# Kernel tuning notes

Hardware: AMD Instinct MI355X
Metric: run time of the kernel (lower is better)

Reference implementation:

```python
import jax, jax.numpy as jnp
import numpy as np

F = 256          # in_features
T = 8            # num_fragment_ion_types = 4 types * 2 charges
N_MONO, N_CLEAV, N_FRAG, N_OUT = 150000, 100000, 80000, 40000
D_CLEAV, D_JOIN, D_COMB = 4, 2, 4


def setup_inputs() -> dict:
    key = jax.random.key(0)
    ks = jax.random.split(key, 14)
    s = 0.05
    return {
        "feature": jax.random.normal(ks[0], (N_MONO, F), jnp.float32),
        "Wg_lost": jax.random.normal(ks[1], (F, 1), jnp.float32) * s,
        "Wg_ret": jax.random.normal(ks[2], (F, 1), jnp.float32) * s,
        "W_ih": jax.random.normal(ks[3], (4 * F, 2 * F), jnp.float32) * s,
        "W_hh": jax.random.normal(ks[4], (4 * F, F), jnp.float32) * s,
        "b_ih": jax.random.normal(ks[5], (4 * F,), jnp.float32) * s,
        "b_hh": jax.random.normal(ks[6], (4 * F,), jnp.float32) * s,
        "Wg_frag": jax.random.normal(ks[7], (F, 1), jnp.float32) * s,
        "W_out": jax.random.normal(ks[8], (F, T), jnp.float32) * s,
        "b_out": jnp.zeros((T,), jnp.float32),
        "lost_src": jax.random.randint(ks[9], (N_CLEAV, D_CLEAV), 0, N_MONO),
        "retained_src": jax.random.randint(ks[10], (N_CLEAV, D_CLEAV), 0, N_MONO),
        "join_src": jax.random.randint(ks[11], (N_FRAG, D_JOIN), 0, N_CLEAV),
        "combine_src": jax.random.randint(ks[12], (N_OUT, D_COMB), 0, N_FRAG),
    }


def _attention_sum(h, Wg):
    # h: [N, D, F] mailbox; gate = Linear(F,1,no bias); softmax over neighbor axis
    logits = jnp.einsum('ndf,fo->ndo', h, Wg)          # [N, D, 1]
    a = jax.nn.softmax(logits, axis=1)
    return jnp.sum(a * h, axis=1)                       # [N, F]


def _lstm(x, W_ih, W_hh, b_ih, b_hh):
    # x: [N, L, I]; torch nn.LSTM gate order i,f,g,o; zero initial state
    N = x.shape[0]
    H = W_hh.shape[1]
    def step(carry, xt):
        h, c = carry
        gates = xt @ W_ih.T + h @ W_hh.T + b_ih + b_hh  # [N, 4H]
        i, f, g, o = jnp.split(gates, 4, axis=-1)
        c = jax.nn.sigmoid(f) * c + jax.nn.sigmoid(i) * jnp.tanh(g)
        h = jax.nn.sigmoid(o) * jnp.tanh(c)
        return (h, c), h
    init = (jnp.zeros((N, H), x.dtype), jnp.zeros((N, H), x.dtype))
    _, hs = jax.lax.scan(step, init, jnp.swapaxes(x, 0, 1))
    return jnp.swapaxes(hs, 0, 1)                       # [N, L, H]


def reference(feature, Wg_lost, Wg_ret, W_ih, W_hh, b_ih, b_hh,
              Wg_frag, W_out, b_out,
              lost_src, retained_src, join_src, combine_src):
    h_lost = _attention_sum(feature[lost_src], Wg_lost)        # [N_cleav, F]
    h_ret = _attention_sum(feature[retained_src], Wg_ret)      # [N_cleav, F]
    cleav = jnp.concatenate([h_lost, h_ret], axis=-1)          # [N_cleav, 2F]
    # Fragment pull over 'join' edges: LSTM over neighbor set, then attention sum
    hs = _lstm(cleav[join_src], W_ih, W_hh, b_ih, b_hh)        # [N_frag, D_join, F]
    frag = _attention_sum(hs, Wg_frag)                         # [N_frag, F]
    # Output head: Linear + ReLU
    frag_out = jax.nn.relu(frag @ W_out + b_out)               # [N_frag, T]
    # copy_u_sum over 'combine' edges: scatter-sum of src outputs to dst
    return frag_out[combine_src].sum(axis=1)                   # [N_out, T]
```

## Files before the change

### kernel.cpp

```cpp
#include <hip/hip_runtime.h>

typedef unsigned short u16;
typedef unsigned int u32;
typedef float f32x4 __attribute__((ext_vector_type(4)));
typedef __bf16 bf16x8 __attribute__((ext_vector_type(8)));

#define F 256
#define T_OUT 8
#define N_MONO 150000
#define N_CLEAV 100000
#define N_FRAG 80000
#define N_OUT 40000
#define M_CLEAV_PAD 100352

static __device__ __forceinline__ u16 f2bf(float f) {
  u32 u = __float_as_uint(f);
  u32 r = (u + 0x7FFFu + ((u >> 16) & 1u)) >> 16;
  return (u16)r;
}
static __device__ __forceinline__ float bf2f(u16 b) {
  return __uint_as_float(((u32)b) << 16);
}
static __device__ __forceinline__ float sigmoidf(float x) {
  return __frcp_rn(1.0f + __expf(-x));
}
static __device__ __forceinline__ float fast_tanh(float x) {
  return 1.0f - 2.0f * __frcp_rn(__expf(2.0f * x) + 1.0f);
}
static __device__ __forceinline__ void async_copy16(const u16* g, const u16* l) {
  __builtin_amdgcn_global_load_lds(
      (const __attribute__((address_space(1))) u32*)g,
      (__attribute__((address_space(3))) u32*)l,
      16, 0, 0);
}

__global__ __launch_bounds__(256) void prep_kernel(
    const float* __restrict__ Wih, const float* __restrict__ Whh,
    const float* __restrict__ bih, const float* __restrict__ bhh,
    u16* __restrict__ Wihb, u16* __restrict__ Whhb, float* __restrict__ bias) {
  int i = blockIdx.x * 256 + threadIdx.x;
  if (i < 1024 * 512) Wihb[i] = f2bf(Wih[i]);
  if (i < 1024 * 256) Whhb[i] = f2bf(Whh[i]);
  if (i < 1024) bias[i] = bih[i] + bhh[i];
}

__global__ __launch_bounds__(256) void attn_pull(
    const float* __restrict__ feat, const float* __restrict__ WgL,
    const float* __restrict__ WgR, const int* __restrict__ lostS,
    const int* __restrict__ retS, u16* __restrict__ cleav) {
  int wave = threadIdx.x >> 6, lane = threadIdx.x & 63;
  int n = blockIdx.x * 4 + wave;
  if (n >= N_CLEAV) return;
  const float4 wgl = *(const float4*)(WgL + lane * 4);
  const float4 wgr = *(const float4*)(WgR + lane * 4);
  for (int sg = 0; sg < 2; ++sg) {
    const int* src = sg ? retS : lostS;
    float4 wg = sg ? wgr : wgl;
    int4 ridx = *(const int4*)(src + n * 4);
    int r[4] = {ridx.x, ridx.y, ridx.z, ridx.w};
    float4 x[4];
#pragma unroll
    for (int d = 0; d < 4; ++d)
      x[d] = *(const float4*)(feat + (size_t)r[d] * F + lane * 4);
    float logit[4];
#pragma unroll
    for (int d = 0; d < 4; ++d) {
      float p = x[d].x * wg.x + x[d].y * wg.y + x[d].z * wg.z + x[d].w * wg.w;
#pragma unroll
      for (int off = 32; off; off >>= 1) p += __shfl_xor(p, off);
      logit[d] = p;
    }
    float mx = fmaxf(fmaxf(logit[0], logit[1]), fmaxf(logit[2], logit[3]));
    float e0 = __expf(logit[0] - mx), e1 = __expf(logit[1] - mx);
    float e2 = __expf(logit[2] - mx), e3 = __expf(logit[3] - mx);
    float inv = 1.f / (e0 + e1 + e2 + e3);
    float a0 = e0 * inv, a1 = e1 * inv, a2 = e2 * inv, a3 = e3 * inv;
    float4 acc;
    acc.x = a0 * x[0].x + a1 * x[1].x + a2 * x[2].x + a3 * x[3].x;
    acc.y = a0 * x[0].y + a1 * x[1].y + a2 * x[2].y + a3 * x[3].y;
    acc.z = a0 * x[0].z + a1 * x[1].z + a2 * x[2].z + a3 * x[3].z;
    acc.w = a0 * x[0].w + a1 * x[1].w + a2 * x[2].w + a3 * x[3].w;
    u32 lo = (u32)f2bf(acc.x) | ((u32)f2bf(acc.y) << 16);
    u32 hi = (u32)f2bf(acc.z) | ((u32)f2bf(acc.w) << 16);
    *(uint2*)(cleav + (size_t)n * 512 + sg * 256 + lane * 4) = make_uint2(lo, hi);
  }
}

template <int EPI, int K>
__global__ __launch_bounds__(512, 2) void gemm256(
    const u16* __restrict__ A, const u16* __restrict__ Bw,
    u16* __restrict__ C, const float* __restrict__ bias,
    int nper, int mstrips_valid) {
  __shared__ u16 sh[2][32768];
  const int flat = blockIdx.x;
  const int xcd = flat & 7;
  const int w = flat >> 3;
  const int mstrip = xcd * nper + (w >> 2);
  const int nstrip = w & 3;
  if (mstrip >= mstrips_valid) return;
  const int m0 = mstrip * 256;
  const int n0 = nstrip * 256;

  const int tid = threadIdx.x;
  const int lane = tid & 63;
  const int wave = tid >> 6;
  const int quad = lane >> 4;
  const int l16 = lane & 15;
  const int s7 = l16 & 7;
  const int wm2 = wave >> 2;
  const int wn4 = wave & 3;

  const int arow = (wm2 * 128 + l16) * 64;
  const int brow = 16384 + (wn4 * 64 + l16) * 64;
  const int coff0 = ((0 + quad) ^ s7) * 8;
  const int coff1 = ((4 + quad) ^ s7) * 8;

  int srow[2], ssw[2], sdst[2];
#pragma unroll
  for (int j = 0; j < 2; j++) {
    int c = j * 512 + tid;
    int r = c >> 3, p = c & 7;
    srow[j] = r;
    ssw[j] = (p ^ (r & 7)) * 8;
    sdst[j] = (j * 512 + (tid & ~63)) * 8;
  }
  const u16* Abase = A + (size_t)m0 * K;
  const u16* Bbase = Bw + (size_t)n0 * K;

  auto stage = [&](int buf, int mat, int h, int kt) {
    const u16* gb = (mat ? Bbase : Abase) + (size_t)(h * 128) * K + kt * 64;
    const u16* lb = &sh[buf][mat * 16384 + h * 8192];
#pragma unroll
    for (int j = 0; j < 2; j++)
      async_copy16(gb + (size_t)srow[j] * K + ssw[j], lb + sdst[j]);
  };

  f32x4 acc[8][4];
#pragma unroll
  for (int i = 0; i < 8; i++)
#pragma unroll
    for (int j = 0; j < 4; j++) acc[i][j] = (f32x4){0.f, 0.f, 0.f, 0.f};

  constexpr int nK = K / 64;
  stage(0, 0, 0, 0); stage(0, 0, 1, 0); stage(0, 1, 0, 0); stage(0, 1, 1, 0);
  if (nK > 1) { stage(1, 1, 0, 1); stage(1, 1, 1, 1); }
  __builtin_amdgcn_s_waitcnt(0xF74);
  __builtin_amdgcn_s_barrier();

  bf16x8 a[4][2], b0[2][2], b1[2][2];
#pragma unroll
  for (int t = 0; t < nK; ++t) {
    const int bsel = t & 1;
    const u16* S = &sh[bsel][0];

#pragma unroll
    for (int i = 0; i < 4; i++) {
      a[i][0] = *(const bf16x8*)&S[arow + i * 1024 + coff0];
      a[i][1] = *(const bf16x8*)&S[arow + i * 1024 + coff1];
    }
#pragma unroll
    for (int j = 0; j < 2; j++) {
      b0[j][0] = *(const bf16x8*)&S[brow + j * 1024 + coff0];
      b0[j][1] = *(const bf16x8*)&S[brow + j * 1024 + coff1];
    }
    if (t + 1 < nK) stage(bsel ^ 1, 0, 0, t + 1);
    __builtin_amdgcn_s_waitcnt(0xC87F);
    __builtin_amdgcn_s_barrier();
    __builtin_amdgcn_s_waitcnt(0xC07F);
    __builtin_amdgcn_sched_barrier(0);
    __builtin_amdgcn_s_setprio(1);
#pragma unroll
    for (int i = 0; i < 4; i++)
#pragma unroll
      for (int j = 0; j < 2; j++) {
        acc[i][j] = __builtin_amdgcn_mfma_f32_16x16x32_bf16(a[i][0], b0[j][0], acc[i][j], 0, 0, 0);
        acc[i][j] = __builtin_amdgcn_mfma_f32_16x16x32_bf16(a[i][1], b0[j][1], acc[i][j], 0, 0, 0);
      }
    __builtin_amdgcn_s_setprio(0);
    __builtin_amdgcn_s_barrier();

#pragma unroll
    for (int j = 0; j < 2; j++) {
      b1[j][0] = *(const bf16x8*)&S[brow + (2 + j) * 1024 + coff0];
      b1[j][1] = *(const bf16x8*)&S[brow + (2 + j) * 1024 + coff1];
    }
    if (t + 1 < nK) stage(bsel ^ 1, 0, 1, t + 1);
    __builtin_amdgcn_s_barrier();
    __builtin_amdgcn_s_waitcnt(0xC07F);
    __builtin_amdgcn_sched_barrier(0);
    __builtin_amdgcn_s_setprio(1);
#pragma unroll
    for (int i = 0; i < 4; i++)
#pragma unroll
      for (int j = 0; j < 2; j++) {
        acc[i][2 + j] = __builtin_amdgcn_mfma_f32_16x16x32_bf16(a[i][0], b1[j][0], acc[i][2 + j], 0, 0, 0);
        acc[i][2 + j] = __builtin_amdgcn_mfma_f32_16x16x32_bf16(a[i][1], b1[j][1], acc[i][2 + j], 0, 0, 0);
      }
    __builtin_amdgcn_s_setprio(0);
    __builtin_amdgcn_s_barrier();

#pragma unroll
    for (int i = 0; i < 4; i++) {
      a[i][0] = *(const bf16x8*)&S[arow + (4 + i) * 1024 + coff0];
      a[i][1] = *(const bf16x8*)&S[arow + (4 + i) * 1024 + coff1];
    }
    if (t + 2 < nK) stage(bsel, 1, 0, t + 2);
    __builtin_amdgcn_s_barrier();
    __builtin_amdgcn_s_waitcnt(0xC07F);
    __builtin_amdgcn_sched_barrier(0);
    __builtin_amdgcn_s_setprio(1);
#pragma unroll
    for (int i = 0; i < 4; i++)
#pragma unroll
      for (int j = 0; j < 2; j++) {
        acc[4 + i][j] = __builtin_amdgcn_mfma_f32_16x16x32_bf16(a[i][0], b0[j][0], acc[4 + i][j], 0, 0, 0);
        acc[4 + i][j] = __builtin_amdgcn_mfma_f32_16x16x32_bf16(a[i][1], b0[j][1], acc[4 + i][j], 0, 0, 0);
      }
    __builtin_amdgcn_s_setprio(0);
    __builtin_amdgcn_s_barrier();

    if (t + 2 < nK) stage(bsel, 1, 1, t + 2);
    __builtin_amdgcn_s_barrier();
    __builtin_amdgcn_s_setprio(1);
#pragma unroll
    for (int i = 0; i < 4; i++)
#pragma unroll
      for (int j = 0; j < 2; j++) {
        acc[4 + i][2 + j] = __builtin_amdgcn_mfma_f32_16x16x32_bf16(a[i][0], b1[j][0], acc[4 + i][2 + j], 0, 0, 0);
        acc[4 + i][2 + j] = __builtin_amdgcn_mfma_f32_16x16x32_bf16(a[i][1], b1[j][1], acc[4 + i][2 + j], 0, 0, 0);
      }
    __builtin_amdgcn_s_setprio(0);
    if (t + 2 < nK) __builtin_amdgcn_s_waitcnt(0xF74);
    else            __builtin_amdgcn_s_waitcnt(0xF70);
    __builtin_amdgcn_s_barrier();
  }

  float badd[4];
#pragma unroll
  for (int j = 0; j < 4; j++)
    badd[j] = (EPI == 0) ? bias[n0 + wn4 * 64 + j * 16 + l16] : 0.f;
#pragma unroll
  for (int i = 0; i < 8; i++) {
    const int mrow = m0 + wm2 * 128 + i * 16 + quad * 4;
#pragma unroll
    for (int j = 0; j < 4; j++) {
      const int n = n0 + wn4 * 64 + j * 16 + l16;
#pragma unroll
      for (int r = 0; r < 4; r++)
        C[(size_t)(mrow + r) * 1024 + n] = f2bf(acc[i][j][r] + badd[j]);
    }
  }
}

__global__ __launch_bounds__(256) void lstm_step1(
    const u16* __restrict__ P, const int* __restrict__ join,
    u16* __restrict__ h1, u16* __restrict__ c1) {
  int wave = threadIdx.x >> 6, lane = threadIdx.x & 63;
  int m = blockIdx.x * 4 + wave;
  if (m >= N_FRAG) return;
  int j0 = join[2 * m];
  const u16* row = P + (size_t)j0 * 1024 + lane * 4;
  ushort4 iv = *(const ushort4*)(row);
  ushort4 gv = *(const ushort4*)(row + 512);
  ushort4 ov = *(const ushort4*)(row + 768);
  const u16* ivp = (const u16*)&iv;
  const u16* gvp = (const u16*)&gv;
  const u16* ovp = (const u16*)&ov;
  ushort4 h4, c4;
  u16* h4p = (u16*)&h4;
  u16* c4p = (u16*)&c4;
#pragma unroll
  for (int k = 0; k < 4; k++) {
    float c = sigmoidf(bf2f(ivp[k])) * fast_tanh(bf2f(gvp[k]));
    float hv = sigmoidf(bf2f(ovp[k])) * fast_tanh(c);
    h4p[k] = f2bf(hv);
    c4p[k] = f2bf(c);
  }
  *(ushort4*)(h1 + (size_t)m * 256 + lane * 4) = h4;
  *(ushort4*)(c1 + (size_t)m * 256 + lane * 4) = c4;
}

__global__ __launch_bounds__(256) void lstm_step2_attn_out(
    const u16* __restrict__ G2, const u16* __restrict__ P,
    const int* __restrict__ join, const u16* __restrict__ c1,
    const u16* __restrict__ h1b, const float* __restrict__ Wg,
    const float* __restrict__ Wout, const float* __restrict__ bout,
    float* __restrict__ frag_out) {
  int wave = threadIdx.x >> 6, lane = threadIdx.x & 63;
  int m = blockIdx.x * 4 + wave;
  if (m >= N_FRAG) return;
  int j1 = join[2 * m + 1];
  const u16* row = G2 + (size_t)m * 1024 + lane * 4;
  const u16* prow = P + (size_t)j1 * 1024 + lane * 4;
  ushort4 iv = *(const ushort4*)(row);
  ushort4 fv = *(const ushort4*)(row + 256);
  ushort4 gv = *(const ushort4*)(row + 512);
  ushort4 ov = *(const ushort4*)(row + 768);
  ushort4 pi = *(const ushort4*)(prow);
  ushort4 pf = *(const ushort4*)(prow + 256);
  ushort4 pg = *(const ushort4*)(prow + 512);
  ushort4 po = *(const ushort4*)(prow + 768);
  ushort4 c4 = *(const ushort4*)(c1 + (size_t)m * 256 + lane * 4);
  ushort4 h4 = *(const ushort4*)(h1b + (size_t)m * 256 + lane * 4);
  float4 wg = *(const float4*)(Wg + lane * 4);
  const u16* ivp = (const u16*)&iv; const u16* pip = (const u16*)&pi;
  const u16* fvp = (const u16*)&fv; const u16* pfp = (const u16*)&pf;
  const u16* gvp = (const u16*)&gv; const u16* pgp = (const u16*)&pg;
  const u16* ovp = (const u16*)&ov; const u16* pop = (const u16*)&po;
  const u16* c4p = (const u16*)&c4;
  const u16* h4p = (const u16*)&h4;
  const float* wgp = (const float*)&wg;

  float h1v[4], h2v[4];
  float p1 = 0.f, p2 = 0.f;
#pragma unroll
  for (int k = 0; k < 4; k++) {
    float gi = bf2f(ivp[k]) + bf2f(pip[k]);
    float gf = bf2f(fvp[k]) + bf2f(pfp[k]);
    float gg = bf2f(gvp[k]) + bf2f(pgp[k]);
    float go = bf2f(ovp[k]) + bf2f(pop[k]);
    float c2 = sigmoidf(gf) * bf2f(c4p[k]) + sigmoidf(gi) * fast_tanh(gg);
    float h2 = sigmoidf(go) * fast_tanh(c2);
    h2v[k] = h2;
    h1v[k] = bf2f(h4p[k]);
    p1 += h1v[k] * wgp[k];
    p2 += h2 * wgp[k];
  }
#pragma unroll
  for (int off = 32; off; off >>= 1) {
    p1 += __shfl_xor(p1, off);
    p2 += __shfl_xor(p2, off);
  }
  float mx = fmaxf(p1, p2);
  float e1 = __expf(p1 - mx), e2 = __expf(p2 - mx);
  float inv = __frcp_rn(e1 + e2);
  float a1 = e1 * inv, a2 = e2 * inv;

  float acc[8];
#pragma unroll
  for (int t = 0; t < 8; t++) acc[t] = 0.f;
#pragma unroll
  for (int k = 0; k < 4; k++) {
    float frag = a1 * h1v[k] + a2 * h2v[k];
    int h = lane * 4 + k;
    float4 w0 = *(const float4*)(Wout + h * 8);
    float4 w1 = *(const float4*)(Wout + h * 8 + 4);
    acc[0] += frag * w0.x; acc[1] += frag * w0.y;
    acc[2] += frag * w0.z; acc[3] += frag * w0.w;
    acc[4] += frag * w1.x; acc[5] += frag * w1.y;
    acc[6] += frag * w1.z; acc[7] += frag * w1.w;
  }
#pragma unroll
  for (int off = 32; off; off >>= 1)
#pragma unroll
    for (int t = 0; t < 8; t++) acc[t] += __shfl_xor(acc[t], off);
  if (lane == 0) {
    float4 o0, o1;
    o0.x = fmaxf(acc[0] + bout[0], 0.f);
    o0.y = fmaxf(acc[1] + bout[1], 0.f);
    o0.z = fmaxf(acc[2] + bout[2], 0.f);
    o0.w = fmaxf(acc[3] + bout[3], 0.f);
    o1.x = fmaxf(acc[4] + bout[4], 0.f);
    o1.y = fmaxf(acc[5] + bout[5], 0.f);
    o1.z = fmaxf(acc[6] + bout[6], 0.f);
    o1.w = fmaxf(acc[7] + bout[7], 0.f);
    *(float4*)(frag_out + (size_t)m * 8) = o0;
    *(float4*)(frag_out + (size_t)m * 8 + 4) = o1;
  }
}

__global__ __launch_bounds__(256) void scatter_sum(
    const float* __restrict__ frag_out, const int* __restrict__ comb,
    float* __restrict__ out) {
  int tid = blockIdx.x * 256 + threadIdx.x;
  if (tid >= N_OUT * 8) return;
  int n = tid >> 3, t = tid & 7;
  float s = 0.f;
#pragma unroll
  for (int d = 0; d < 4; d++) {
    int f = comb[n * 4 + d];
    s += frag_out[(size_t)f * 8 + t];
  }
  out[tid] = s;
}

extern "C" void kernel_launch(void* const* d_in, const int* in_sizes, int n_in,
                              void* d_out, int out_size, void* d_ws, size_t ws_size,
                              hipStream_t stream) {
  const float* feature = (const float*)d_in[0];
  const float* WgL = (const float*)d_in[1];
  const float* WgR = (const float*)d_in[2];
  const float* Wih = (const float*)d_in[3];
  const float* Whh = (const float*)d_in[4];
  const float* bih = (const float*)d_in[5];
  const float* bhh = (const float*)d_in[6];
  const float* Wgf = (const float*)d_in[7];
  const float* Wout = (const float*)d_in[8];
  const float* bout = (const float*)d_in[9];
  const int* lostS = (const int*)d_in[10];
  const int* retS = (const int*)d_in[11];
  const int* joinS = (const int*)d_in[12];
  const int* combS = (const int*)d_in[13];
  float* out = (float*)d_out;

  char* ws = (char*)d_ws;
  size_t off = 0;
  auto alloc = [&](size_t bytes) -> char* {
    char* p = ws + off;
    off = (off + bytes + 255) & ~(size_t)255;
    return p;
  };
  u16* Wihb = (u16*)alloc((size_t)1024 * 512 * 2);
  u16* Whhb = (u16*)alloc((size_t)1024 * 256 * 2);
  float* bias = (float*)alloc(1024 * 4);
  u16* P = (u16*)alloc((size_t)M_CLEAV_PAD * 1024 * 2);
  u16* h1 = (u16*)alloc((size_t)N_FRAG * 256 * 2);
  u16* c1 = (u16*)alloc((size_t)N_FRAG * 256 * 2);
  float* frag_out = (float*)alloc((size_t)N_FRAG * 8 * 4);
  char* uni = alloc((size_t)M_CLEAV_PAD * 1024 * 2);
  u16* cleav = (u16*)uni;
  u16* gates2 = (u16*)uni;

  prep_kernel<<<2048, 256, 0, stream>>>(Wih, Whh, bih, bhh, Wihb, Whhb, bias);
  attn_pull<<<N_CLEAV / 4, 256, 0, stream>>>(feature, WgL, WgR, lostS, retS, cleav);
  gemm256<0, 512><<<1568, 512, 0, stream>>>(cleav, Wihb, P, bias, 49, 392);
  lstm_step1<<<N_FRAG / 4, 256, 0, stream>>>(P, joinS, h1, c1);
  gemm256<1, 256><<<1280, 512, 0, stream>>>(h1, Whhb, gates2, nullptr, 40, 313);
  lstm_step2_attn_out<<<N_FRAG / 4, 256, 0, stream>>>(
      gates2, P, joinS, c1, h1, Wgf, Wout, bout, frag_out);
  scatter_sum<<<(N_OUT * 8 + 255) / 256, 256, 0, stream>>>(frag_out, combS, out);
}
```

Baseline: 683.5 us.

## Precompute per-node gate logits and bf16 feature copy before attention gather

```diff
diff --git a/kernel.cpp b/kernel.cpp
--- a/kernel.cpp
+++ b/kernel.cpp
@@ -44,44 +44,65 @@
   if (i < 1024) bias[i] = bih[i] + bhh[i];
 }
 
-__global__ __launch_bounds__(256) void attn_pull(
+__global__ __launch_bounds__(256) void feat_prep(
     const float* __restrict__ feat, const float* __restrict__ WgL,
-    const float* __restrict__ WgR, const int* __restrict__ lostS,
-    const int* __restrict__ retS, u16* __restrict__ cleav) {
+    const float* __restrict__ WgR, u16* __restrict__ featb,
+    float* __restrict__ glog) {
+  int wave = threadIdx.x >> 6, lane = threadIdx.x & 63;
+  int n = blockIdx.x * 4 + wave;
+  if (n >= N_MONO) return;
+  float4 x = *(const float4*)(feat + (size_t)n * F + lane * 4);
+  u32 lo = (u32)f2bf(x.x) | ((u32)f2bf(x.y) << 16);
+  u32 hi = (u32)f2bf(x.z) | ((u32)f2bf(x.w) << 16);
+  *(uint2*)(featb + (size_t)n * F + lane * 4) = make_uint2(lo, hi);
+  float4 wl = *(const float4*)(WgL + lane * 4);
+  float4 wr = *(const float4*)(WgR + lane * 4);
+  float pl = x.x * wl.x + x.y * wl.y + x.z * wl.z + x.w * wl.w;
+  float pr = x.x * wr.x + x.y * wr.y + x.z * wr.z + x.w * wr.w;
+#pragma unroll
+  for (int off = 32; off; off >>= 1) {
+    pl += __shfl_xor(pl, off);
+    pr += __shfl_xor(pr, off);
+  }
+  if (lane == 0) {
+    glog[n * 2] = pl;
+    glog[n * 2 + 1] = pr;
+  }
+}
+
+__global__ __launch_bounds__(256) void attn_pull2(
+    const u16* __restrict__ featb, const float* __restrict__ glog,
+    const int* __restrict__ lostS, const int* __restrict__ retS,
+    u16* __restrict__ cleav) {
   int wave = threadIdx.x >> 6, lane = threadIdx.x & 63;
   int n = blockIdx.x * 4 + wave;
   if (n >= N_CLEAV) return;
-  const float4 wgl = *(const float4*)(WgL + lane * 4);
-  const float4 wgr = *(const float4*)(WgR + lane * 4);
+#pragma unroll
   for (int sg = 0; sg < 2; ++sg) {
     const int* src = sg ? retS : lostS;
-    float4 wg = sg ? wgr : wgl;
     int4 ridx = *(const int4*)(src + n * 4);
     int r[4] = {ridx.x, ridx.y, ridx.z, ridx.w};
-    float4 x[4];
-#pragma unroll
-    for (int d = 0; d < 4; ++d)
-      x[d] = *(const float4*)(feat + (size_t)r[d] * F + lane * 4);
-    float logit[4];
+    ushort4 x4[4];
+    float lg[4];
 #pragma unroll
     for (int d = 0; d < 4; ++d) {
-      float p = x[d].x * wg.x + x[d].y * wg.y + x[d].z * wg.z + x[d].w * wg.w;
-#pragma unroll
-      for (int off = 32; off; off >>= 1) p += __shfl_xor(p, off);
-      logit[d] = p;
-    }
-    float mx = fmaxf(fmaxf(logit[0], logit[1]), fmaxf(logit[2], logit[3]));
-    float e0 = __expf(logit[0] - mx), e1 = __expf(logit[1] - mx);
-    float e2 = __expf(logit[2] - mx), e3 = __expf(logit[3] - mx);
-    float inv = 1.f / (e0 + e1 + e2 + e3);
-    float a0 = e0 * inv, a1 = e1 * inv, a2 = e2 * inv, a3 = e3 * inv;
-    float4 acc;
-    acc.x = a0 * x[0].x + a1 * x[1].x + a2 * x[2].x + a3 * x[3].x;
-    acc.y = a0 * x[0].y + a1 * x[1].y + a2 * x[2].y + a3 * x[3].y;
-    acc.z = a0 * x[0].z + a1 * x[1].z + a2 * x[2].z + a3 * x[3].z;
-    acc.w = a0 * x[0].w + a1 * x[1].w + a2 * x[2].w + a3 * x[3].w;
-    u32 lo = (u32)f2bf(acc.x) | ((u32)f2bf(acc.y) << 16);
-    u32 hi = (u32)f2bf(acc.z) | ((u32)f2bf(acc.w) << 16);
+      x4[d] = *(const ushort4*)(featb + (size_t)r[d] * F + lane * 4);
+      lg[d] = glog[r[d] * 2 + sg];
+    }
+    float mx = fmaxf(fmaxf(lg[0], lg[1]), fmaxf(lg[2], lg[3]));
+    float e0 = __expf(lg[0] - mx), e1 = __expf(lg[1] - mx);
+    float e2 = __expf(lg[2] - mx), e3 = __expf(lg[3] - mx);
+    float inv = __frcp_rn(e0 + e1 + e2 + e3);
+    float a[4] = {e0 * inv, e1 * inv, e2 * inv, e3 * inv};
+    float acc[4] = {0.f, 0.f, 0.f, 0.f};
+#pragma unroll
+    for (int d = 0; d < 4; ++d) {
+      const u16* xp = (const u16*)&x4[d];
+#pragma unroll
+      for (int k = 0; k < 4; k++) acc[k] += a[d] * bf2f(xp[k]);
+    }
+    u32 lo = (u32)f2bf(acc[0]) | ((u32)f2bf(acc[1]) << 16);
+    u32 hi = (u32)f2bf(acc[2]) | ((u32)f2bf(acc[3]) << 16);
     *(uint2*)(cleav + (size_t)n * 512 + sg * 256 + lane * 4) = make_uint2(lo, hi);
   }
 }
@@ -420,9 +441,12 @@
   char* uni = alloc((size_t)M_CLEAV_PAD * 1024 * 2);
   u16* cleav = (u16*)uni;
   u16* gates2 = (u16*)uni;
+  u16* featb = P;
+  float* glog = (float*)(P + (size_t)N_MONO * F);
 
   prep_kernel<<<2048, 256, 0, stream>>>(Wih, Whh, bih, bhh, Wihb, Whhb, bias);
-  attn_pull<<<N_CLEAV / 4, 256, 0, stream>>>(feature, WgL, WgR, lostS, retS, cleav);
+  feat_prep<<<(N_MONO + 3) / 4, 256, 0, stream>>>(feature, WgL, WgR, featb, glog);
+  attn_pull2<<<N_CLEAV / 4, 256, 0, stream>>>(featb, glog, lostS, retS, cleav);
   gemm256<0, 512><<<1568, 512, 0, stream>>>(cleav, Wihb, P, bias, 49, 392);
   lstm_step1<<<N_FRAG / 4, 256, 0, stream>>>(P, joinS, h1, c1);
   gemm256<1, 256><<<1280, 512, 0, stream>>>(h1, Whhb, gates2, nullptr, 40, 313);
```

New measurement: 659.5 us. 3.5% less time.
